# Performance work log

Hardware: AMD Instinct MI355X
Metric: run time of the kernel (lower is better)

Reference implementation:

```python
import jax, jax.numpy as jnp
import numpy as np

SCALE = 1.0 / np.float32(64.0 ** 0.5)  # module hard-codes sqrt(64), not sqrt(d)


def setup_inputs() -> dict:
    key = jax.random.key(0)
    k1, k2 = jax.random.split(key)
    x = jax.random.normal(k1, (8, 2048, 1024), dtype=jnp.float32)
    kernel = jax.random.normal(k2, (3, 1024, 1024), dtype=jnp.float32) * 0.02
    return {"x": x, "kernel": kernel}


def reference(x, kernel):
    # x: [B, S, D], kernel: [3, D, O]
    wq = jnp.einsum('bsd,do->bso', x, kernel[0])
    wk = jnp.einsum('bsd,do->bso', x, kernel[1])
    wv = jnp.einsum('bsd,do->bso', x, kernel[2])
    scores = jnp.einsum('bqo,bko->bqk', wq, wk) * SCALE  # [B, S, S]
    attn = jax.nn.softmax(scores, axis=-1)
    return jnp.einsum('bqk,bko->bqo', attn, wv)  # [B, S, O]
```

## Files before the change

kernel.cpp:

```cpp
#include <hip/hip_runtime.h>

typedef _Float16 f16;
typedef f16 f16x8 __attribute__((ext_vector_type(8)));
typedef f16 f16x4 __attribute__((ext_vector_type(4)));
typedef float f32x4 __attribute__((ext_vector_type(4)));

#define GLD_LDS16(g, l) __builtin_amdgcn_global_load_lds( \
    (const __attribute__((address_space(1))) void*)(g),   \
    (__attribute__((address_space(3))) void*)(l), 16, 0, 0)

__device__ __forceinline__ void bar() {
    asm volatile("" ::: "memory");
    __builtin_amdgcn_s_barrier();
    asm volatile("" ::: "memory");
}
#define WAIT_VM(n) { asm volatile("s_waitcnt vmcnt(" #n ")" ::: "memory"); \
                     __builtin_amdgcn_sched_barrier(0); }
#define LGKM(n)    { asm volatile("s_waitcnt lgkmcnt(" #n ")" ::: "memory"); \
                     __builtin_amdgcn_sched_barrier(0); }

__global__ __launch_bounds__(256) void cast_x_kernel(const float* __restrict__ x,
                                                     f16* __restrict__ xh) {
    long i = ((long)blockIdx.x * 256 + threadIdx.x) * 8;
    float4 a = *(const float4*)&x[i];
    float4 b = *(const float4*)&x[i + 4];
    f16x8 v;
    v[0] = (f16)a.x; v[1] = (f16)a.y; v[2] = (f16)a.z; v[3] = (f16)a.w;
    v[4] = (f16)b.x; v[5] = (f16)b.y; v[6] = (f16)b.z; v[7] = (f16)b.w;
    *(f16x8*)&xh[i] = v;
}

__global__ __launch_bounds__(256) void cast_transpose_w(const float* __restrict__ W,
                                                        f16* __restrict__ WT) {
    __shared__ float tile[64][65];
    const int iz = blockIdx.z;
    const int d0 = blockIdx.y * 64;
    const int o0 = blockIdx.x * 64;
    const float* Wi = W + (long)iz * 1024 * 1024;
    f16* WTi = WT + (long)iz * 1024 * 1024;
    const int t = threadIdx.x;
#pragma unroll
    for (int j = 0; j < 4; ++j) {
        int idx = t + j * 256;
        int r = idx >> 4;
        int c4 = (idx & 15) * 4;
        float4 v = *(const float4*)&Wi[(long)(d0 + r) * 1024 + o0 + c4];
        tile[r][c4 + 0] = v.x; tile[r][c4 + 1] = v.y;
        tile[r][c4 + 2] = v.z; tile[r][c4 + 3] = v.w;
    }
    __syncthreads();
#pragma unroll
    for (int j = 0; j < 2; ++j) {
        int idx = t + j * 256;
        int ol = idx >> 3;
        int c8 = (idx & 7) * 8;
        f16x8 v;
#pragma unroll
        for (int e = 0; e < 8; ++e) v[e] = (f16)tile[c8 + e][ol];
        *(f16x8*)&WTi[(long)(o0 + ol) * 1024 + d0 + c8] = v;
    }
}

template <int MODE>
__global__ __launch_bounds__(512, 2)
void gemm256(const f16* __restrict__ A, const f16* __restrict__ B,
             void* __restrict__ Cv, const float* __restrict__ dinv,
             int lda, int ldb, int K,
             long sA, long sB, long sC, int ldc, float scale) {
    extern __shared__ __align__(16) char smem[];
    const int tid = threadIdx.x;
    const int lane = tid & 63;
    const int wave = tid >> 6;
    const int wm = wave >> 2;
    const int wn = wave & 3;
    const int z = blockIdx.z;

    const int o_ = blockIdx.x + gridDim.x * blockIdx.y;
    const int nwg = gridDim.x * gridDim.y;
    const int sw = (o_ & 7) * (nwg >> 3) + (o_ >> 3);
    const int bx = sw % gridDim.x;
    const int by = sw / gridDim.x;

    const long m_base = (long)by * 256;
    const long n_base = (long)bx * 256;
    const f16* Ab = A + (long)z * sA;
    const f16* Bb = B + (long)z * sB;

    const int c_r0 = tid >> 3;
    const int c_col = ((tid & 7) * 8) ^ ((c_r0 & 7) << 3);
    const long oA0 = (m_base + c_r0) * (long)lda + c_col;
    const long oA1 = oA0 + 64L * lda;
    const long oB0 = (n_base + c_r0) * (long)ldb + c_col;
    const long oB1 = oB0 + 64L * ldb;

#define ST_A0(bf_, kt_) { long k0_ = (long)(kt_) * 64; \
    char* d_ = smem + (bf_) * 65536 + tid * 16; \
    GLD_LDS16(Ab + oA0 + k0_, d_); GLD_LDS16(Ab + oA1 + k0_, d_ + 8192); }
#define ST_A1(bf_, kt_) { long k0_ = (long)(kt_) * 64 + 128L * lda; \
    char* d_ = smem + (bf_) * 65536 + 16384 + tid * 16; \
    GLD_LDS16(Ab + oA0 + k0_, d_); GLD_LDS16(Ab + oA1 + k0_, d_ + 8192); }
#define ST_B0(bf_, kt_) { long k0_ = (long)(kt_) * 64; \
    char* d_ = smem + (bf_) * 65536 + 32768 + tid * 16; \
    GLD_LDS16(Bb + oB0 + k0_, d_); GLD_LDS16(Bb + oB1 + k0_, d_ + 8192); }
#define ST_B1(bf_, kt_) { long k0_ = (long)(kt_) * 64 + 128L * ldb; \
    char* d_ = smem + (bf_) * 65536 + 49152 + tid * 16; \
    GLD_LDS16(Bb + oB0 + k0_, d_); GLD_LDS16(Bb + oB1 + k0_, d_ + 8192); }

    const int fr = lane & 15;
    const int rq = lane >> 4;
    const int cs0 = (rq * 16) ^ ((lane & 7) << 4);
    const int cs1 = cs0 ^ 64;
    const int aoff = wm * 16384 + fr * 128;
    const int boff = 32768 + (wn >> 1) * 16384 + (wn & 1) * 8192 + fr * 128;

    f32x4 acc[8][4];
#pragma unroll
    for (int i = 0; i < 8; ++i)
#pragma unroll
        for (int j = 0; j < 4; ++j) acc[i][j] = (f32x4){0.f, 0.f, 0.f, 0.f};

    const int NT = K >> 6;

    ST_B0(0, 0); ST_B1(0, 0); ST_A0(0, 0); ST_A1(0, 0);
    WAIT_VM(4);
    ST_B0(1, 1); ST_B1(1, 1); ST_A0(1, 1);
    WAIT_VM(6);
    bar();

    for (int j = 0; j < NT; ++j) {
        char* bufb = smem + (j & 1) * 65536;
        const char* Ap = bufb + aoff;
        const char* Bp = bufb + boff;
        f16x8 af[4][2], bf[4][2];

#pragma unroll
        for (int i = 0; i < 4; ++i) {
            af[i][0] = *(const f16x8*)(Ap + i * 2048 + cs0);
            af[i][1] = *(const f16x8*)(Ap + i * 2048 + cs1);
        }
        __builtin_amdgcn_sched_barrier(0);
#pragma unroll
        for (int ni = 0; ni < 2; ++ni) {
            bf[ni][0] = *(const f16x8*)(Bp + ni * 2048 + cs0);
            bf[ni][1] = *(const f16x8*)(Bp + ni * 2048 + cs1);
        }
        __builtin_amdgcn_sched_barrier(0);
#pragma unroll
        for (int ni = 2; ni < 4; ++ni) {
            bf[ni][0] = *(const f16x8*)(Bp + ni * 2048 + cs0);
            bf[ni][1] = *(const f16x8*)(Bp + ni * 2048 + cs1);
        }
        if (j + 1 < NT) ST_A1((j + 1) & 1, j + 1);
        bar();
        LGKM(4);
        __builtin_amdgcn_s_setprio(1);
#pragma unroll
        for (int ks = 0; ks < 2; ++ks)
#pragma unroll
            for (int i = 0; i < 4; ++i)
#pragma unroll
                for (int n = 0; n < 2; ++n)
                    acc[i][n] = __builtin_amdgcn_mfma_f32_16x16x32_f16(
                        af[i][ks], bf[n][ks], acc[i][n], 0, 0, 0);
        __builtin_amdgcn_s_setprio(0);
        bar();

        LGKM(0);
        if (j + 2 < NT) ST_B0(j & 1, j + 2);
        bar();
        __builtin_amdgcn_s_setprio(1);
#pragma unroll
        for (int ks = 0; ks < 2; ++ks)
#pragma unroll
            for (int i = 0; i < 4; ++i)
#pragma unroll
                for (int n = 0; n < 2; ++n)
                    acc[i][2 + n] = __builtin_amdgcn_mfma_f32_16x16x32_f16(
                        af[i][ks], bf[2 + n][ks], acc[i][2 + n], 0, 0, 0);
        __builtin_amdgcn_s_setprio(0);
        bar();

#pragma unroll
        for (int i = 0; i < 4; ++i) {
            af[i][0] = *(const f16x8*)(Ap + (4 + i) * 2048 + cs0);
            af[i][1] = *(const f16x8*)(Ap + (4 + i) * 2048 + cs1);
        }
        if (j + 2 < NT) ST_B1(j & 1, j + 2);
        bar();
        LGKM(0);
        __builtin_amdgcn_s_setprio(1);
#pragma unroll
        for (int ks = 0; ks < 2; ++ks)
#pragma unroll
            for (int i = 0; i < 4; ++i)
#pragma unroll
                for (int n = 0; n < 2; ++n)
                    acc[4 + i][n] = __builtin_amdgcn_mfma_f32_16x16x32_f16(
                        af[i][ks], bf[n][ks], acc[4 + i][n], 0, 0, 0);
        __builtin_amdgcn_s_setprio(0);
        bar();

        if (j + 2 < NT) {
            ST_A0(j & 1, j + 2);
            WAIT_VM(6);
        } else if (j + 1 < NT) {
            WAIT_VM(0);
        }
        bar();
        __builtin_amdgcn_s_setprio(1);
#pragma unroll
        for (int ks = 0; ks < 2; ++ks)
#pragma unroll
            for (int i = 0; i < 4; ++i)
#pragma unroll
                for (int n = 0; n < 2; ++n)
                    acc[4 + i][2 + n] = __builtin_amdgcn_mfma_f32_16x16x32_f16(
                        af[i][ks], bf[2 + n][ks], acc[4 + i][2 + n], 0, 0, 0);
        __builtin_amdgcn_s_setprio(0);
        bar();
    }

#pragma unroll
    for (int mi = 0; mi < 8; ++mi) {
        long r0 = m_base + wm * 128 + mi * 16 + rq * 4;
#pragma unroll
        for (int ni = 0; ni < 4; ++ni) {
            long c = n_base + wn * 64 + ni * 16 + fr;
            if constexpr (MODE == 0) {
                f16* C = (f16*)Cv + (long)z * sC;
#pragma unroll
                for (int jj = 0; jj < 4; ++jj)
                    C[(r0 + jj) * (long)ldc + c] =
                        (f16)__expf(acc[mi][ni][jj] * scale - 4.0f);
            } else if constexpr (MODE == 2) {
                float* C = (float*)Cv + (long)z * sC;
#pragma unroll
                for (int jj = 0; jj < 4; ++jj)
                    C[(r0 + jj) * (long)ldc + c] =
                        acc[mi][ni][jj] * dinv[(long)z * 2048 + r0 + jj];
            } else {
                f16* W = (f16*)Cv;
                if (c < 2048) {
                    f16* C = W + (c >> 10) * 16777216L + (c & 1023);
#pragma unroll
                    for (int jj = 0; jj < 4; ++jj)
                        C[(r0 + jj) * 1024L] = (f16)acc[mi][ni][jj];
                } else {
                    long o = c - 2048;
                    long b = r0 >> 11;
                    long s = r0 & 2047;
                    f16x4 v;
#pragma unroll
                    for (int jj = 0; jj < 4; ++jj) v[jj] = (f16)acc[mi][ni][jj];
                    *(f16x4*)&W[33554432L + b * 2097152L + o * 2048L + s] = v;
                }
            }
        }
    }
#undef ST_A0
#undef ST_A1
#undef ST_B0
#undef ST_B1
}

__global__ __launch_bounds__(256) void rowsum_inv(const f16* __restrict__ E,
                                                  float* __restrict__ dinv) {
    const f16* p = E + (long)blockIdx.x * 2048;
    const int t = threadIdx.x;
    const int lane = t & 63;
    const int wv = t >> 6;
    __shared__ float red[4];

    f16x8 v = *(const f16x8*)&p[t * 8];
    float s = 0.f;
#pragma unroll
    for (int e = 0; e < 8; ++e) s += (float)v[e];
#pragma unroll
    for (int o = 32; o; o >>= 1) s += __shfl_xor(s, o);
    if (lane == 0) red[wv] = s;
    __syncthreads();
    if (t == 0) dinv[blockIdx.x] = 1.f / (red[0] + red[1] + red[2] + red[3]);
}

extern "C" void kernel_launch(void* const* d_in, const int* in_sizes, int n_in,
                              void* d_out, int out_size, void* d_ws, size_t ws_size,
                              hipStream_t stream) {
    const float* x = (const float*)d_in[0];
    const float* w = (const float*)d_in[1];
    float* out = (float*)d_out;
    char* ws = (char*)d_ws;

    f16* qh = (f16*)(ws + 0);
    f16* kh = (f16*)(ws + 33554432);
    f16* vt = (f16*)(ws + 67108864);
    f16* xh = (f16*)(ws + 100663296);
    f16* wh = (f16*)(ws + 134217728);
    f16* sp = (f16*)(ws + 100663296);
    float* dinv = (float*)(ws + 0);

    cast_x_kernel<<<8192, 256, 0, stream>>>(x, xh);
    cast_transpose_w<<<dim3(16, 16, 3), 256, 0, stream>>>(w, wh);

    gemm256<3><<<dim3(12, 64, 1), 512, 131072, stream>>>(
        xh, wh, ws, nullptr, 1024, 1024, 1024, 0L, 0L, 0L, 0, 1.0f);

    gemm256<0><<<dim3(8, 8, 8), 512, 131072, stream>>>(
        qh, kh, sp, nullptr, 1024, 1024, 1024, 2097152L, 2097152L, 4194304L, 2048, 0.125f);

    rowsum_inv<<<16384, 256, 0, stream>>>(sp, dinv);

    gemm256<2><<<dim3(4, 8, 8), 512, 131072, stream>>>(
        sp, vt, out, dinv, 2048, 2048, 2048, 4194304L, 2097152L, 2097152L, 1024, 1.0f);
}
```

Baseline: 303.1 us.

## Switch GEMMs to 32x32 MFMA and fuse row-sum into score epilogue

Replaces the 16x16x32 MFMA tiling with 32x32x16 MFMA fragments across all three GEMMs. This cuts LDS fragment reads per FLOP and uses fewer, larger matrix instructions. The exp-score GEMM now also produces per-tile partial row sums, via shuffles and LDS, written into the output buffer as scratch. This replaces the separate pass that re-read the full fp16 score matrix with a tiny reduction kernel. The new epilogue stores have a different access pattern and may coalesce worse, and the scratch use of the output buffer adds a hidden dependency.

```diff
diff --git a/kernel.cpp b/kernel.cpp
--- a/kernel.cpp
+++ b/kernel.cpp
@@ -3,7 +3,7 @@
 typedef _Float16 f16;
 typedef f16 f16x8 __attribute__((ext_vector_type(8)));
 typedef f16 f16x4 __attribute__((ext_vector_type(4)));
-typedef float f32x4 __attribute__((ext_vector_type(4)));
+typedef float f32x16 __attribute__((ext_vector_type(16)));
 
 #define GLD_LDS16(g, l) __builtin_amdgcn_global_load_lds( \
     (const __attribute__((address_space(1))) void*)(g),   \
@@ -65,6 +65,7 @@
 __global__ __launch_bounds__(512, 2)
 void gemm256(const f16* __restrict__ A, const f16* __restrict__ B,
              void* __restrict__ Cv, const float* __restrict__ dinv,
+             float* __restrict__ psum,
              int lda, int ldb, int K,
              long sA, long sB, long sC, int ldc, float scale) {
     extern __shared__ __align__(16) char smem[];
@@ -106,18 +107,17 @@
     char* d_ = smem + (bf_) * 65536 + 49152 + tid * 16; \
     GLD_LDS16(Bb + oB0 + k0_, d_); GLD_LDS16(Bb + oB1 + k0_, d_ + 8192); }
 
-    const int fr = lane & 15;
-    const int rq = lane >> 4;
-    const int cs0 = (rq * 16) ^ ((lane & 7) << 4);
-    const int cs1 = cs0 ^ 64;
-    const int aoff = wm * 16384 + fr * 128;
-    const int boff = 32768 + (wn >> 1) * 16384 + (wn & 1) * 8192 + fr * 128;
-
-    f32x4 acc[8][4];
-#pragma unroll
-    for (int i = 0; i < 8; ++i)
-#pragma unroll
-        for (int j = 0; j < 4; ++j) acc[i][j] = (f32x4){0.f, 0.f, 0.f, 0.f};
+    const int l31 = lane & 31;
+    const int kh16 = (lane >> 5) << 4;
+    const int key = (lane & 7) << 4;
+    const int arow = wm * 16384 + l31 * 128;
+    const int brow = 32768 + (wn >> 1) * 16384 + (((wn & 1) << 6) + l31) * 128;
+
+    f32x16 acc[4][2];
+#pragma unroll
+    for (int i = 0; i < 4; ++i)
+#pragma unroll
+        for (int n = 0; n < 2; ++n) acc[i][n] = (f32x16){};
 
     const int NT = K >> 6;
 
@@ -129,39 +129,33 @@
 
     for (int j = 0; j < NT; ++j) {
         char* bufb = smem + (j & 1) * 65536;
-        const char* Ap = bufb + aoff;
-        const char* Bp = bufb + boff;
-        f16x8 af[4][2], bf[4][2];
-
-#pragma unroll
-        for (int i = 0; i < 4; ++i) {
-            af[i][0] = *(const f16x8*)(Ap + i * 2048 + cs0);
-            af[i][1] = *(const f16x8*)(Ap + i * 2048 + cs1);
-        }
+        const char* Ap = bufb + arow;
+        const char* Bp = bufb + brow;
+        f16x8 af[2][4], bf[2][4];
+
+#pragma unroll
+        for (int mf = 0; mf < 2; ++mf)
+#pragma unroll
+            for (int kt = 0; kt < 4; ++kt)
+                af[mf][kt] = *(const f16x8*)(Ap + mf * 4096 + (((kt << 5) | kh16) ^ key));
         __builtin_amdgcn_sched_barrier(0);
 #pragma unroll
-        for (int ni = 0; ni < 2; ++ni) {
-            bf[ni][0] = *(const f16x8*)(Bp + ni * 2048 + cs0);
-            bf[ni][1] = *(const f16x8*)(Bp + ni * 2048 + cs1);
-        }
+        for (int kt = 0; kt < 4; ++kt)
+            bf[0][kt] = *(const f16x8*)(Bp + (((kt << 5) | kh16) ^ key));
         __builtin_amdgcn_sched_barrier(0);
 #pragma unroll
-        for (int ni = 2; ni < 4; ++ni) {
-            bf[ni][0] = *(const f16x8*)(Bp + ni * 2048 + cs0);
-            bf[ni][1] = *(const f16x8*)(Bp + ni * 2048 + cs1);
-        }
+        for (int kt = 0; kt < 4; ++kt)
+            bf[1][kt] = *(const f16x8*)(Bp + 4096 + (((kt << 5) | kh16) ^ key));
         if (j + 1 < NT) ST_A1((j + 1) & 1, j + 1);
         bar();
         LGKM(4);
         __builtin_amdgcn_s_setprio(1);
 #pragma unroll
-        for (int ks = 0; ks < 2; ++ks)
-#pragma unroll
-            for (int i = 0; i < 4; ++i)
-#pragma unroll
-                for (int n = 0; n < 2; ++n)
-                    acc[i][n] = __builtin_amdgcn_mfma_f32_16x16x32_f16(
-                        af[i][ks], bf[n][ks], acc[i][n], 0, 0, 0);
+        for (int kt = 0; kt < 4; ++kt)
+#pragma unroll
+            for (int mf = 0; mf < 2; ++mf)
+                acc[mf][0] = __builtin_amdgcn_mfma_f32_32x32x16_f16(
+                    af[mf][kt], bf[0][kt], acc[mf][0], 0, 0, 0);
         __builtin_amdgcn_s_setprio(0);
         bar();
 
@@ -170,33 +164,29 @@
         bar();
         __builtin_amdgcn_s_setprio(1);
 #pragma unroll
-        for (int ks = 0; ks < 2; ++ks)
-#pragma unroll
-            for (int i = 0; i < 4; ++i)
-#pragma unroll
-                for (int n = 0; n < 2; ++n)
-                    acc[i][2 + n] = __builtin_amdgcn_mfma_f32_16x16x32_f16(
-                        af[i][ks], bf[2 + n][ks], acc[i][2 + n], 0, 0, 0);
+        for (int kt = 0; kt < 4; ++kt)
+#pragma unroll
+            for (int mf = 0; mf < 2; ++mf)
+                acc[mf][1] = __builtin_amdgcn_mfma_f32_32x32x16_f16(
+                    af[mf][kt], bf[1][kt], acc[mf][1], 0, 0, 0);
         __builtin_amdgcn_s_setprio(0);
         bar();
 
 #pragma unroll
-        for (int i = 0; i < 4; ++i) {
-            af[i][0] = *(const f16x8*)(Ap + (4 + i) * 2048 + cs0);
-            af[i][1] = *(const f16x8*)(Ap + (4 + i) * 2048 + cs1);
-        }
+        for (int mf = 0; mf < 2; ++mf)
+#pragma unroll
+            for (int kt = 0; kt < 4; ++kt)
+                af[mf][kt] = *(const f16x8*)(Ap + (2 + mf) * 4096 + (((kt << 5) | kh16) ^ key));
         if (j + 2 < NT) ST_B1(j & 1, j + 2);
         bar();
         LGKM(0);
         __builtin_amdgcn_s_setprio(1);
 #pragma unroll
-        for (int ks = 0; ks < 2; ++ks)
-#pragma unroll
-            for (int i = 0; i < 4; ++i)
-#pragma unroll
-                for (int n = 0; n < 2; ++n)
-                    acc[4 + i][n] = __builtin_amdgcn_mfma_f32_16x16x32_f16(
-                        af[i][ks], bf[n][ks], acc[4 + i][n], 0, 0, 0);
+        for (int kt = 0; kt < 4; ++kt)
+#pragma unroll
+            for (int mf = 0; mf < 2; ++mf)
+                acc[2 + mf][0] = __builtin_amdgcn_mfma_f32_32x32x16_f16(
+                    af[mf][kt], bf[0][kt], acc[2 + mf][0], 0, 0, 0);
         __builtin_amdgcn_s_setprio(0);
         bar();
 
@@ -209,52 +199,98 @@
         bar();
         __builtin_amdgcn_s_setprio(1);
 #pragma unroll
-        for (int ks = 0; ks < 2; ++ks)
-#pragma unroll
-            for (int i = 0; i < 4; ++i)
-#pragma unroll
-                for (int n = 0; n < 2; ++n)
-                    acc[4 + i][2 + n] = __builtin_amdgcn_mfma_f32_16x16x32_f16(
-                        af[i][ks], bf[2 + n][ks], acc[4 + i][2 + n], 0, 0, 0);
+        for (int kt = 0; kt < 4; ++kt)
+#pragma unroll
+            for (int mf = 0; mf < 2; ++mf)
+                acc[2 + mf][1] = __builtin_amdgcn_mfma_f32_32x32x16_f16(
+                    af[mf][kt], bf[1][kt], acc[2 + mf][1], 0, 0, 0);
         __builtin_amdgcn_s_setprio(0);
         bar();
     }
 
-#pragma unroll
-    for (int mi = 0; mi < 8; ++mi) {
-        long r0 = m_base + wm * 128 + mi * 16 + rq * 4;
-#pragma unroll
-        for (int ni = 0; ni < 4; ++ni) {
-            long c = n_base + wn * 64 + ni * 16 + fr;
-            if constexpr (MODE == 0) {
-                f16* C = (f16*)Cv + (long)z * sC;
-#pragma unroll
-                for (int jj = 0; jj < 4; ++jj)
-                    C[(r0 + jj) * (long)ldc + c] =
-                        (f16)__expf(acc[mi][ni][jj] * scale - 4.0f);
-            } else if constexpr (MODE == 2) {
-                float* C = (float*)Cv + (long)z * sC;
-#pragma unroll
-                for (int jj = 0; jj < 4; ++jj)
-                    C[(r0 + jj) * (long)ldc + c] =
-                        acc[mi][ni][jj] * dinv[(long)z * 2048 + r0 + jj];
-            } else {
-                f16* W = (f16*)Cv;
+    const int lh4 = (lane >> 5) * 4;
+#pragma unroll
+    for (int mf = 0; mf < 4; ++mf) {
+        long rbase = m_base + wm * 128 + mf * 32;
+        if constexpr (MODE == 0) {
+            f16* C = (f16*)Cv + (long)z * sC;
+#pragma unroll
+            for (int q = 0; q < 4; ++q) {
+                float p[4] = {0.f, 0.f, 0.f, 0.f};
+#pragma unroll
+                for (int nf = 0; nf < 2; ++nf) {
+                    long c = n_base + wn * 64 + nf * 32 + l31;
+#pragma unroll
+                    for (int jj = 0; jj < 4; ++jj) {
+                        float e = __expf(acc[mf][nf][q * 4 + jj] * scale - 4.0f);
+                        C[(rbase + q * 8 + lh4 + jj) * (long)ldc + c] = (f16)e;
+                        p[jj] += e;
+                    }
+                }
+#pragma unroll
+                for (int jj = 0; jj < 4; ++jj) {
+#pragma unroll
+                    for (int o = 16; o; o >>= 1) p[jj] += __shfl_xor(p[jj], o);
+                }
+                if (l31 == 0) {
+                    float* wsum = (float*)smem;
+                    int rl = wm * 128 + mf * 32 + q * 8 + lh4;
+#pragma unroll
+                    for (int jj = 0; jj < 4; ++jj)
+                        wsum[wn * 256 + rl + jj] = p[jj];
+                }
+            }
+        } else if constexpr (MODE == 2) {
+            float* C = (float*)Cv + (long)z * sC;
+#pragma unroll
+            for (int nf = 0; nf < 2; ++nf) {
+                long c = n_base + wn * 64 + nf * 32 + l31;
+#pragma unroll
+                for (int q = 0; q < 4; ++q)
+#pragma unroll
+                    for (int jj = 0; jj < 4; ++jj) {
+                        long r = rbase + q * 8 + lh4 + jj;
+                        C[r * (long)ldc + c] =
+                            acc[mf][nf][q * 4 + jj] * dinv[(long)z * 2048 + r];
+                    }
+            }
+        } else {
+            f16* W = (f16*)Cv;
+#pragma unroll
+            for (int nf = 0; nf < 2; ++nf) {
+                long c = n_base + wn * 64 + nf * 32 + l31;
                 if (c < 2048) {
                     f16* C = W + (c >> 10) * 16777216L + (c & 1023);
 #pragma unroll
-                    for (int jj = 0; jj < 4; ++jj)
-                        C[(r0 + jj) * 1024L] = (f16)acc[mi][ni][jj];
+                    for (int q = 0; q < 4; ++q)
+#pragma unroll
+                        for (int jj = 0; jj < 4; ++jj)
+                            C[(rbase + q * 8 + lh4 + jj) * 1024L] =
+                                (f16)acc[mf][nf][q * 4 + jj];
                 } else {
                     long o = c - 2048;
-                    long b = r0 >> 11;
-                    long s = r0 & 2047;
-                    f16x4 v;
-#pragma unroll
-                    for (int jj = 0; jj < 4; ++jj) v[jj] = (f16)acc[mi][ni][jj];
-                    *(f16x4*)&W[33554432L + b * 2097152L + o * 2048L + s] = v;
+#pragma unroll
+                    for (int q = 0; q < 4; ++q) {
+                        long r0 = rbase + q * 8 + lh4;
+                        long b = r0 >> 11;
+                        long s = r0 & 2047;
+                        f16x4 v;
+#pragma unroll
+                        for (int jj = 0; jj < 4; ++jj)
+                            v[jj] = (f16)acc[mf][nf][q * 4 + jj];
+                        *(f16x4*)&W[33554432L + b * 2097152L + o * 2048L + s] = v;
+                    }
                 }
             }
+        }
+    }
+
+    if constexpr (MODE == 0) {
+        bar();
+        if (tid < 256) {
+            const float* wsum = (const float*)smem;
+            float s = wsum[tid] + wsum[256 + tid] + wsum[512 + tid] + wsum[768 + tid];
+            psum[((long)z * 2048 + m_base + tid) * 8 + bx] = s;
         }
     }
 #undef ST_A0
@@ -263,23 +299,12 @@
 #undef ST_B1
 }
 
-__global__ __launch_bounds__(256) void rowsum_inv(const f16* __restrict__ E,
-                                                  float* __restrict__ dinv) {
-    const f16* p = E + (long)blockIdx.x * 2048;
-    const int t = threadIdx.x;
-    const int lane = t & 63;
-    const int wv = t >> 6;
-    __shared__ float red[4];
-
-    f16x8 v = *(const f16x8*)&p[t * 8];
-    float s = 0.f;
-#pragma unroll
-    for (int e = 0; e < 8; ++e) s += (float)v[e];
-#pragma unroll
-    for (int o = 32; o; o >>= 1) s += __shfl_xor(s, o);
-    if (lane == 0) red[wv] = s;
-    __syncthreads();
-    if (t == 0) dinv[blockIdx.x] = 1.f / (red[0] + red[1] + red[2] + red[3]);
+__global__ __launch_bounds__(256) void reduce_dinv(const float* __restrict__ psum,
+                                                   float* __restrict__ dinv) {
+    int r = blockIdx.x * 256 + threadIdx.x;
+    float4 a = *(const float4*)&psum[(long)r * 8];
+    float4 b = *(const float4*)&psum[(long)r * 8 + 4];
+    dinv[r] = 1.f / (a.x + a.y + a.z + a.w + b.x + b.y + b.z + b.w);
 }
 
 extern "C" void kernel_launch(void* const* d_in, const int* in_sizes, int n_in,
@@ -297,18 +322,19 @@
     f16* wh = (f16*)(ws + 134217728);
     f16* sp = (f16*)(ws + 100663296);
     float* dinv = (float*)(ws + 0);
+    float* psum = (float*)d_out;
 
     cast_x_kernel<<<8192, 256, 0, stream>>>(x, xh);
     cast_transpose_w<<<dim3(16, 16, 3), 256, 0, stream>>>(w, wh);
 
     gemm256<3><<<dim3(12, 64, 1), 512, 131072, stream>>>(
-        xh, wh, ws, nullptr, 1024, 1024, 1024, 0L, 0L, 0L, 0, 1.0f);
+        xh, wh, ws, nullptr, nullptr, 1024, 1024, 1024, 0L, 0L, 0L, 0, 1.0f);
 
     gemm256<0><<<dim3(8, 8, 8), 512, 131072, stream>>>(
-        qh, kh, sp, nullptr, 1024, 1024, 1024, 2097152L, 2097152L, 4194304L, 2048, 0.125f);
-
-    rowsum_inv<<<16384, 256, 0, stream>>>(sp, dinv);
+        qh, kh, sp, nullptr, psum, 1024, 1024, 1024, 2097152L, 2097152L, 4194304L, 2048, 0.125f);
+
+    reduce_dinv<<<64, 256, 0, stream>>>(psum, dinv);
 
     gemm256<2><<<dim3(4, 8, 8), 512, 131072, stream>>>(
-        sp, vt, out, dinv, 2048, 2048, 2048, 4194304L, 2097152L, 2097152L, 1024, 1.0f);
-}
+        sp, vt, out, dinv, nullptr, 2048, 2048, 2048, 4194304L, 2097152L, 2097152L, 1024, 1.0f);
+}
```

Result: slower. 341.2 us (+12.6%).

## Fold Wq·Wkᵀ into one weight matrix and fuse row-sum into the exp GEMM

Applied to the files above, without the earlier changes.

Scores are computed as x·(Wq Wkᵀ)·xᵀ: a small 1024x1024 GEMM builds the combined weight, and the projection GEMM then produces only T = x·M and Vᵀ rather than Q and K, which shrinks the projection GEMM from 3072 to 2048 output columns. The exp-score GEMM now reduces partial row sums in registers, shuffles and LDS and writes them to a scratch buffer. A tiny kernel combines those sums into the inverse normalisers, replacing the separate pass that re-read the whole score matrix. In exchange the score GEMM's second operand becomes x, an extra small GEMM launch is added, and the fp16 rounding of the precombined weight changes numerical error.

```diff
diff --git a/kernel.cpp b/kernel.cpp
--- a/kernel.cpp
+++ b/kernel.cpp
@@ -19,8 +19,8 @@
 #define LGKM(n)    { asm volatile("s_waitcnt lgkmcnt(" #n ")" ::: "memory"); \
                      __builtin_amdgcn_sched_barrier(0); }
 
-__global__ __launch_bounds__(256) void cast_x_kernel(const float* __restrict__ x,
-                                                     f16* __restrict__ xh) {
+__global__ __launch_bounds__(256) void cast_f32_f16(const float* __restrict__ x,
+                                                    f16* __restrict__ xh) {
     long i = ((long)blockIdx.x * 256 + threadIdx.x) * 8;
     float4 a = *(const float4*)&x[i];
     float4 b = *(const float4*)&x[i + 4];
@@ -30,14 +30,11 @@
     *(f16x8*)&xh[i] = v;
 }
 
-__global__ __launch_bounds__(256) void cast_transpose_w(const float* __restrict__ W,
-                                                        f16* __restrict__ WT) {
+__global__ __launch_bounds__(256) void cast_transpose_1k(const float* __restrict__ Wi,
+                                                         f16* __restrict__ WTi) {
     __shared__ float tile[64][65];
-    const int iz = blockIdx.z;
     const int d0 = blockIdx.y * 64;
     const int o0 = blockIdx.x * 64;
-    const float* Wi = W + (long)iz * 1024 * 1024;
-    f16* WTi = WT + (long)iz * 1024 * 1024;
     const int t = threadIdx.x;
 #pragma unroll
     for (int j = 0; j < 4; ++j) {
@@ -65,6 +62,7 @@
 __global__ __launch_bounds__(512, 2)
 void gemm256(const f16* __restrict__ A, const f16* __restrict__ B,
              void* __restrict__ Cv, const float* __restrict__ dinv,
+             float* __restrict__ psum,
              int lda, int ldb, int K,
              long sA, long sB, long sC, int ldc, float scale) {
     extern __shared__ __align__(16) char smem[];
@@ -220,39 +218,81 @@
         bar();
     }
 
-#pragma unroll
-    for (int mi = 0; mi < 8; ++mi) {
-        long r0 = m_base + wm * 128 + mi * 16 + rq * 4;
-#pragma unroll
-        for (int ni = 0; ni < 4; ++ni) {
-            long c = n_base + wn * 64 + ni * 16 + fr;
-            if constexpr (MODE == 0) {
-                f16* C = (f16*)Cv + (long)z * sC;
+    if constexpr (MODE == 0) {
+        f16* C = (f16*)Cv + (long)z * sC;
+        float p[8][4];
+#pragma unroll
+        for (int mi = 0; mi < 8; ++mi)
+#pragma unroll
+            for (int jj = 0; jj < 4; ++jj) p[mi][jj] = 0.f;
+#pragma unroll
+        for (int mi = 0; mi < 8; ++mi) {
+            long r0 = m_base + wm * 128 + mi * 16 + rq * 4;
+#pragma unroll
+            for (int ni = 0; ni < 4; ++ni) {
+                long c = n_base + wn * 64 + ni * 16 + fr;
+#pragma unroll
+                for (int jj = 0; jj < 4; ++jj) {
+                    float e = __expf(acc[mi][ni][jj] * scale - 4.0f);
+                    C[(r0 + jj) * (long)ldc + c] = (f16)e;
+                    p[mi][jj] += e;
+                }
+            }
+        }
+#pragma unroll
+        for (int mi = 0; mi < 8; ++mi)
+#pragma unroll
+            for (int jj = 0; jj < 4; ++jj)
+#pragma unroll
+                for (int o = 8; o; o >>= 1)
+                    p[mi][jj] += __shfl_xor(p[mi][jj], o);
+        float* wsum = (float*)smem;
+        if (fr == 0) {
+#pragma unroll
+            for (int mi = 0; mi < 8; ++mi)
 #pragma unroll
                 for (int jj = 0; jj < 4; ++jj)
-                    C[(r0 + jj) * (long)ldc + c] =
-                        (f16)__expf(acc[mi][ni][jj] * scale - 4.0f);
-            } else if constexpr (MODE == 2) {
-                float* C = (float*)Cv + (long)z * sC;
-#pragma unroll
-                for (int jj = 0; jj < 4; ++jj)
-                    C[(r0 + jj) * (long)ldc + c] =
-                        acc[mi][ni][jj] * dinv[(long)z * 2048 + r0 + jj];
-            } else {
-                f16* W = (f16*)Cv;
-                if (c < 2048) {
-                    f16* C = W + (c >> 10) * 16777216L + (c & 1023);
+                    wsum[wn * 256 + wm * 128 + mi * 16 + rq * 4 + jj] = p[mi][jj];
+        }
+        bar();
+        if (tid < 256) {
+            float s = wsum[tid] + wsum[256 + tid] + wsum[512 + tid] + wsum[768 + tid];
+            psum[((long)z * 2048 + m_base + tid) * 8 + bx] = s;
+        }
+    } else {
+#pragma unroll
+        for (int mi = 0; mi < 8; ++mi) {
+            long r0 = m_base + wm * 128 + mi * 16 + rq * 4;
+#pragma unroll
+            for (int ni = 0; ni < 4; ++ni) {
+                long c = n_base + wn * 64 + ni * 16 + fr;
+                if constexpr (MODE == 1) {
+                    f16* C = (f16*)Cv + (long)z * sC;
 #pragma unroll
                     for (int jj = 0; jj < 4; ++jj)
-                        C[(r0 + jj) * 1024L] = (f16)acc[mi][ni][jj];
+                        C[(r0 + jj) * (long)ldc + c] = (f16)(acc[mi][ni][jj] * scale);
+                } else if constexpr (MODE == 2) {
+                    float* C = (float*)Cv + (long)z * sC;
+#pragma unroll
+                    for (int jj = 0; jj < 4; ++jj)
+                        C[(r0 + jj) * (long)ldc + c] =
+                            acc[mi][ni][jj] * dinv[(long)z * 2048 + r0 + jj];
                 } else {
-                    long o = c - 2048;
-                    long b = r0 >> 11;
-                    long s = r0 & 2047;
-                    f16x4 v;
-#pragma unroll
-                    for (int jj = 0; jj < 4; ++jj) v[jj] = (f16)acc[mi][ni][jj];
-                    *(f16x4*)&W[33554432L + b * 2097152L + o * 2048L + s] = v;
+                    if (c < 1024) {
+                        f16* T = (f16*)Cv;
+#pragma unroll
+                        for (int jj = 0; jj < 4; ++jj)
+                            T[(r0 + jj) * 1024L + c] = (f16)acc[mi][ni][jj];
+                    } else {
+                        f16* VT = (f16*)((char*)Cv + 67108864);
+                        long o = c - 1024;
+                        long b = r0 >> 11;
+                        long s = r0 & 2047;
+                        f16x4 v;
+#pragma unroll
+                        for (int jj = 0; jj < 4; ++jj) v[jj] = (f16)acc[mi][ni][jj];
+                        *(f16x4*)&VT[b * 2097152L + o * 2048L + s] = v;
+                    }
                 }
             }
         }
@@ -263,23 +303,12 @@
 #undef ST_B1
 }
 
-__global__ __launch_bounds__(256) void rowsum_inv(const f16* __restrict__ E,
-                                                  float* __restrict__ dinv) {
-    const f16* p = E + (long)blockIdx.x * 2048;
-    const int t = threadIdx.x;
-    const int lane = t & 63;
-    const int wv = t >> 6;
-    __shared__ float red[4];
-
-    f16x8 v = *(const f16x8*)&p[t * 8];
-    float s = 0.f;
-#pragma unroll
-    for (int e = 0; e < 8; ++e) s += (float)v[e];
-#pragma unroll
-    for (int o = 32; o; o >>= 1) s += __shfl_xor(s, o);
-    if (lane == 0) red[wv] = s;
-    __syncthreads();
-    if (t == 0) dinv[blockIdx.x] = 1.f / (red[0] + red[1] + red[2] + red[3]);
+__global__ __launch_bounds__(256) void reduce_dinv(const float* __restrict__ psum,
+                                                   float* __restrict__ dinv) {
+    int r = blockIdx.x * 256 + threadIdx.x;
+    float4 a = *(const float4*)&psum[(long)r * 8];
+    float4 b = *(const float4*)&psum[(long)r * 8 + 4];
+    dinv[r] = 1.f / (a.x + a.y + a.z + a.w + b.x + b.y + b.z + b.w);
 }
 
 extern "C" void kernel_launch(void* const* d_in, const int* in_sizes, int n_in,
@@ -290,25 +319,34 @@
     float* out = (float*)d_out;
     char* ws = (char*)d_ws;
 
-    f16* qh = (f16*)(ws + 0);
-    f16* kh = (f16*)(ws + 33554432);
-    f16* vt = (f16*)(ws + 67108864);
-    f16* xh = (f16*)(ws + 100663296);
-    f16* wh = (f16*)(ws + 134217728);
-    f16* sp = (f16*)(ws + 100663296);
+    f16* th  = (f16*)(ws + 0);
+    f16* xh  = (f16*)(ws + 33554432);
+    f16* vt  = (f16*)(ws + 67108864);
+    char* spB = ws + 100663296;
+    f16* whq = (f16*)(spB);
+    f16* whk = (f16*)(spB + 2097152);
+    f16* bTV = (f16*)(spB + 4194304);
+    f16* sp  = (f16*)(spB);
     float* dinv = (float*)(ws + 0);
-
-    cast_x_kernel<<<8192, 256, 0, stream>>>(x, xh);
-    cast_transpose_w<<<dim3(16, 16, 3), 256, 0, stream>>>(w, wh);
-
-    gemm256<3><<<dim3(12, 64, 1), 512, 131072, stream>>>(
-        xh, wh, ws, nullptr, 1024, 1024, 1024, 0L, 0L, 0L, 0, 1.0f);
+    float* psum = (float*)d_out;
+
+    cast_f32_f16<<<1024, 256, 0, stream>>>(w, whq);
+    cast_transpose_1k<<<dim3(16, 16), 256, 0, stream>>>(w + 2097152, bTV + 1048576);
+    cast_f32_f16<<<8192, 256, 0, stream>>>(x, xh);
+
+    gemm256<1><<<dim3(4, 4, 1), 512, 131072, stream>>>(
+        whk, whq, bTV, nullptr, nullptr, 1024, 1024, 1024, 0L, 0L, 0L, 1024, 1.0f);
+
+    gemm256<4><<<dim3(8, 64, 1), 512, 131072, stream>>>(
+        xh, bTV, ws, nullptr, nullptr, 1024, 1024, 1024, 0L, 0L, 0L, 0, 1.0f);
 
     gemm256<0><<<dim3(8, 8, 8), 512, 131072, stream>>>(
-        qh, kh, sp, nullptr, 1024, 1024, 1024, 2097152L, 2097152L, 4194304L, 2048, 0.125f);
-
-    rowsum_inv<<<16384, 256, 0, stream>>>(sp, dinv);
+        th, xh, sp, nullptr, psum, 1024, 1024, 1024,
+        2097152L, 2097152L, 4194304L, 2048, 0.125f);
+
+    reduce_dinv<<<64, 256, 0, stream>>>(psum, dinv);
 
     gemm256<2><<<dim3(4, 8, 8), 512, 131072, stream>>>(
-        sp, vt, out, dinv, 2048, 2048, 2048, 4194304L, 2097152L, 2097152L, 1024, 1.0f);
-}
+        sp, vt, out, dinv, nullptr, 2048, 2048, 2048,
+        4194304L, 2097152L, 2097152L, 1024, 1.0f);
+}
```

Measured after the change: 295.6 us. -2.5%, faster.
